# Kernel optimization log

Hardware: AMD Instinct MI355X
Metric: run time of the kernel (lower is better)

The kernel has to match this reference:

```python
import jax, jax.numpy as jnp
import numpy as np

NEI_SIZE = [16]  # matches init kwarg nei_size

def setup_inputs() -> dict:
    key = jax.random.key(0)
    k = jax.random.split(key, 5)
    B, N, S = 512, 32, 16
    EF, NF = 64, 128
    return {
        "x": jax.random.normal(k[0], (B, N, NF), dtype=jnp.float32),
        "x_nei_rel": jax.random.normal(k[1], (B, N * S, EF), dtype=jnp.float32),
        "x_nei_node": jax.random.normal(k[2], (B, N * S, NF), dtype=jnp.float32),
        "W1_w": jax.random.normal(k[3], (NF, EF + NF), dtype=jnp.float32) * 0.05,
        "W1_b": jax.random.normal(k[4], (NF,), dtype=jnp.float32) * 0.05,
        "i": 0,
    }

def reference(x, x_nei_rel, x_nei_node, W1_w, W1_b, i):
    S = NEI_SIZE[i]                       # now_nei_size (static python int)
    B, N, D = x.shape                     # N = n_neibor, D = nodeFea
    norm = 1.0 / np.sqrt(D).astype(np.float32)
    # concat edge+node feats and project: [B, N*S, EF+NF] -> [B, N*S, D]
    x_nei = jnp.concatenate([x_nei_rel, x_nei_node], axis=-1)
    v = (x_nei @ W1_w.T + W1_b).reshape(B, N, S, D)
    # per-node attention over its S neighbors
    alpha = jnp.einsum('bnd,bnsd->bns', x, v) * norm   # [B, N, S]
    alpha = jax.nn.softmax(alpha, axis=-1)
    # weighted neighbor sum
    return jnp.einsum('bns,bnsd->bnd', alpha, v)       # [B, N, D]
```

## Files before the change

### kernel.cpp

```cpp
#include <hip/hip_runtime.h>
#include <stdint.h>


typedef __attribute__((ext_vector_type(8))) short short8;
typedef __attribute__((ext_vector_type(4))) float float4_t;
typedef __attribute__((ext_vector_type(4))) unsigned short ushort4_t;

#define NBLK 2048
#define TILES_PER_BLK 8

__device__ __forceinline__ unsigned short f2bf(float f) {
    uint32_t u = __float_as_uint(f);
    u += 0x7fffu + ((u >> 16) & 1u);
    return (unsigned short)(u >> 16);
}

__device__ __forceinline__ int aoff(int s, int kc) {
    return (((kc >> 5) * 64) + (((kc & 31) >> 3) * 16) + s) * 8 + (kc & 7);
}

__global__ __launch_bounds__(128, 3) void nei_attn_kernel(
    const float* __restrict__ x,
    const float* __restrict__ rel,
    const float* __restrict__ node,
    const float* __restrict__ W,
    const float* __restrict__ bias,
    float* __restrict__ out)
{
    __shared__ __align__(16) unsigned short lds_f[6 * 64 * 8];
    __shared__ __align__(16) float lds_v[16][132];
    __shared__ float lds_alpha[2][16];
    __shared__ float lds_w[2][16];

    const int t    = threadIdx.x;
    const int lane = t & 63;
    const int wv   = t >> 6;
    const int l15  = lane & 15;
    const int quad = lane >> 4;

    short8 wfrag[4][6];
    #pragma unroll
    for (int dt = 0; dt < 4; ++dt) {
        const float* wr = W + (size_t)(64 * wv + dt * 16 + l15) * 192;
        #pragma unroll
        for (int q = 0; q < 6; ++q) {
            const float* p = wr + q * 32 + quad * 8;
            float4_t a = *(const float4_t*)p;
            float4_t b = *(const float4_t*)(p + 4);
            short8 f;
            f[0] = (short)f2bf(a.x); f[1] = (short)f2bf(a.y);
            f[2] = (short)f2bf(a.z); f[3] = (short)f2bf(a.w);
            f[4] = (short)f2bf(b.x); f[5] = (short)f2bf(b.y);
            f[6] = (short)f2bf(b.z); f[7] = (short)f2bf(b.w);
            wfrag[dt][q] = f;
        }
    }
    const float bias_l = bias[64 * wv + lane];

    const int s_st = wv * 8 + (lane & 7);
    const int fb   = lane >> 3;
    int ao[6];
    #pragma unroll
    for (int c = 0; c < 6; ++c) ao[c] = aoff(s_st, (fb + 8 * c) * 4);

    int tile = blockIdx.x * TILES_PER_BLK;
    for (int it = 0; it < TILES_PER_BLK; ++it, ++tile) {
        float4_t ld[6];
        {
            const float4_t* rb = (const float4_t*)rel  + (size_t)tile * 256 + s_st * 16;
            const float4_t* nb = (const float4_t*)node + (size_t)tile * 512 + s_st * 32;
            ld[0] = rb[fb];      ld[1] = rb[fb + 8];
            ld[2] = nb[fb];      ld[3] = nb[fb + 8];
            ld[4] = nb[fb + 16]; ld[5] = nb[fb + 24];
        }
        #pragma unroll
        for (int c = 0; c < 6; ++c) {
            ushort4_t u;
            u[0] = f2bf(ld[c].x); u[1] = f2bf(ld[c].y);
            u[2] = f2bf(ld[c].z); u[3] = f2bf(ld[c].w);
            *(ushort4_t*)&lds_f[ao[c]] = u;
        }
        __syncthreads();

        float4_t xv[4];
        #pragma unroll
        for (int dt = 0; dt < 4; ++dt)
            xv[dt] = *(const float4_t*)(x + (size_t)tile * 128 + 64 * wv + 16 * dt + 4 * quad);

        float4_t acc[4];
        #pragma unroll
        for (int dt = 0; dt < 4; ++dt) acc[dt] = (float4_t){0.f, 0.f, 0.f, 0.f};
        #pragma unroll
        for (int q = 0; q < 6; ++q) {
            short8 bfr = *(const short8*)&lds_f[(q * 64 + lane) * 8];
            #pragma unroll
            for (int dt = 0; dt < 4; ++dt)
                acc[dt] = __builtin_amdgcn_mfma_f32_16x16x32_bf16(wfrag[dt][q], bfr, acc[dt], 0, 0, 0);
        }

        float ap = 0.f;
        #pragma unroll
        for (int dt = 0; dt < 4; ++dt)
            ap += xv[dt].x * acc[dt][0] + xv[dt].y * acc[dt][1]
                + xv[dt].z * acc[dt][2] + xv[dt].w * acc[dt][3];
        ap += __shfl_xor(ap, 16);
        ap += __shfl_xor(ap, 32);
        if (lane < 16) lds_alpha[wv][lane] = ap;

        #pragma unroll
        for (int dt = 0; dt < 4; ++dt)
            *(float4_t*)&lds_v[l15][64 * wv + 16 * dt + 4 * quad] = acc[dt];

        __syncthreads();

        const float alpha = (ap + lds_alpha[1 - wv][l15]) * 0.08838834764831845f;
        float mx = alpha;
        mx = fmaxf(mx, __shfl_xor(mx, 1));
        mx = fmaxf(mx, __shfl_xor(mx, 2));
        mx = fmaxf(mx, __shfl_xor(mx, 4));
        mx = fmaxf(mx, __shfl_xor(mx, 8));
        const float e = __expf(alpha - mx);
        float den = e;
        den += __shfl_xor(den, 1);
        den += __shfl_xor(den, 2);
        den += __shfl_xor(den, 4);
        den += __shfl_xor(den, 8);
        const float wgt = e / den;
        if (quad == 0) lds_w[wv][l15] = wgt;

        const int md = 64 * wv + lane;
        float4_t w0 = *(const float4_t*)&lds_w[wv][0];
        float4_t w1 = *(const float4_t*)&lds_w[wv][4];
        float4_t w2 = *(const float4_t*)&lds_w[wv][8];
        float4_t w3 = *(const float4_t*)&lds_w[wv][12];
        float o = bias_l;
        o += w0.x * lds_v[0][md]  + w0.y * lds_v[1][md]
           + w0.z * lds_v[2][md]  + w0.w * lds_v[3][md];
        o += w1.x * lds_v[4][md]  + w1.y * lds_v[5][md]
           + w1.z * lds_v[6][md]  + w1.w * lds_v[7][md];
        o += w2.x * lds_v[8][md]  + w2.y * lds_v[9][md]
           + w2.z * lds_v[10][md] + w2.w * lds_v[11][md];
        o += w3.x * lds_v[12][md] + w3.y * lds_v[13][md]
           + w3.z * lds_v[14][md] + w3.w * lds_v[15][md];
        out[(size_t)tile * 128 + md] = o;
    }
}

extern "C" void kernel_launch(void* const* d_in, const int* in_sizes, int n_in,
                              void* d_out, int out_size, void* d_ws, size_t ws_size,
                              hipStream_t stream) {
    const float* x    = (const float*)d_in[0];
    const float* rel  = (const float*)d_in[1];
    const float* node = (const float*)d_in[2];
    const float* W    = (const float*)d_in[3];
    const float* bias = (const float*)d_in[4];
    float* out = (float*)d_out;
    hipLaunchKernelGGL(nei_attn_kernel, dim3(NBLK), dim3(128), 0, stream,
                       x, rel, node, W, bias, out);
}
```

Baseline: 299.7 us.

## Load MFMA B operands directly from global, prefetch next tile, use 4 waves

Drops the LDS staging of converted neighbour features. Each lane now loads its MFMA B fragment straight from global memory and converts it to bf16 in registers with packed conversion intrinsics. The block grows to 4 waves, each owning 32 output dims, which halves the per-thread W fragments and lets more waves hide latency. The next tile's loads are issued after the barrier, and LDS buffers are double-buffered to overlap memory with the softmax and weighted sum, at the cost of more live registers and one fewer barrier per tile.

```diff
diff --git a/kernel.cpp b/kernel.cpp
--- a/kernel.cpp
+++ b/kernel.cpp
@@ -1,25 +1,22 @@
 #include <hip/hip_runtime.h>
+#include <hip/hip_bf16.h>
 #include <stdint.h>
 
 
 typedef __attribute__((ext_vector_type(8))) short short8;
 typedef __attribute__((ext_vector_type(4))) float float4_t;
-typedef __attribute__((ext_vector_type(4))) unsigned short ushort4_t;
 
 #define NBLK 2048
 #define TILES_PER_BLK 8
 
-__device__ __forceinline__ unsigned short f2bf(float f) {
-    uint32_t u = __float_as_uint(f);
-    u += 0x7fffu + ((u >> 16) & 1u);
-    return (unsigned short)(u >> 16);
+__device__ __forceinline__ uint32_t pk2bf(float a, float b) {
+    __hip_bfloat162 h = __float22bfloat162_rn(float2{a, b});
+    union { __hip_bfloat162 h2; uint32_t u; } c;
+    c.h2 = h;
+    return c.u;
 }
 
-__device__ __forceinline__ int aoff(int s, int kc) {
-    return (((kc >> 5) * 64) + (((kc & 31) >> 3) * 16) + s) * 8 + (kc & 7);
-}
-
-__global__ __launch_bounds__(128, 3) void nei_attn_kernel(
+__global__ __launch_bounds__(256, 4) void nei_attn_kernel(
     const float* __restrict__ x,
     const float* __restrict__ rel,
     const float* __restrict__ node,
@@ -27,10 +24,9 @@
     const float* __restrict__ bias,
     float* __restrict__ out)
 {
-    __shared__ __align__(16) unsigned short lds_f[6 * 64 * 8];
-    __shared__ __align__(16) float lds_v[16][132];
-    __shared__ float lds_alpha[2][16];
-    __shared__ float lds_w[2][16];
+    __shared__ __align__(16) float lds_v[2][16][132];
+    __shared__ __align__(16) float lds_alpha[2][16][4];
+    __shared__ __align__(16) float lds_wgt[2][4][16];
 
     const int t    = threadIdx.x;
     const int lane = t & 63;
@@ -38,82 +34,81 @@
     const int l15  = lane & 15;
     const int quad = lane >> 4;
 
-    short8 wfrag[4][6];
+    short8 wfrag[2][6];
     #pragma unroll
-    for (int dt = 0; dt < 4; ++dt) {
-        const float* wr = W + (size_t)(64 * wv + dt * 16 + l15) * 192;
+    for (int dt = 0; dt < 2; ++dt) {
+        const float* wr = W + (size_t)(32 * wv + 16 * dt + l15) * 192 + quad * 8;
         #pragma unroll
         for (int q = 0; q < 6; ++q) {
-            const float* p = wr + q * 32 + quad * 8;
-            float4_t a = *(const float4_t*)p;
-            float4_t b = *(const float4_t*)(p + 4);
-            short8 f;
-            f[0] = (short)f2bf(a.x); f[1] = (short)f2bf(a.y);
-            f[2] = (short)f2bf(a.z); f[3] = (short)f2bf(a.w);
-            f[4] = (short)f2bf(b.x); f[5] = (short)f2bf(b.y);
-            f[6] = (short)f2bf(b.z); f[7] = (short)f2bf(b.w);
-            wfrag[dt][q] = f;
+            float4_t a = *(const float4_t*)(wr + 32 * q);
+            float4_t b = *(const float4_t*)(wr + 32 * q + 4);
+            union { uint32_t u[4]; short8 s; } f;
+            f.u[0] = pk2bf(a.x, a.y); f.u[1] = pk2bf(a.z, a.w);
+            f.u[2] = pk2bf(b.x, b.y); f.u[3] = pk2bf(b.z, b.w);
+            wfrag[dt][q] = f.s;
         }
     }
-    const float bias_l = bias[64 * wv + lane];
-
-    const int s_st = wv * 8 + (lane & 7);
-    const int fb   = lane >> 3;
-    int ao[6];
-    #pragma unroll
-    for (int c = 0; c < 6; ++c) ao[c] = aoff(s_st, (fb + 8 * c) * 4);
+    const float bias_l = bias[32 * wv + (lane & 31)];
 
     int tile = blockIdx.x * TILES_PER_BLK;
-    for (int it = 0; it < TILES_PER_BLK; ++it, ++tile) {
-        float4_t ld[6];
-        {
-            const float4_t* rb = (const float4_t*)rel  + (size_t)tile * 256 + s_st * 16;
-            const float4_t* nb = (const float4_t*)node + (size_t)tile * 512 + s_st * 32;
-            ld[0] = rb[fb];      ld[1] = rb[fb + 8];
-            ld[2] = nb[fb];      ld[3] = nb[fb + 8];
-            ld[4] = nb[fb + 16]; ld[5] = nb[fb + 24];
-        }
-        #pragma unroll
-        for (int c = 0; c < 6; ++c) {
-            ushort4_t u;
-            u[0] = f2bf(ld[c].x); u[1] = f2bf(ld[c].y);
-            u[2] = f2bf(ld[c].z); u[3] = f2bf(ld[c].w);
-            *(ushort4_t*)&lds_f[ao[c]] = u;
-        }
-        __syncthreads();
 
-        float4_t xv[4];
-        #pragma unroll
-        for (int dt = 0; dt < 4; ++dt)
-            xv[dt] = *(const float4_t*)(x + (size_t)tile * 128 + 64 * wv + 16 * dt + 4 * quad);
+    float4_t lda[6], ldb[6], xv0, xv1;
+    {
+        const float* fr = rel  + (size_t)tile * 1024 + l15 * 64  + quad * 8;
+        const float* fn = node + (size_t)tile * 2048 + l15 * 128 + quad * 8;
+        lda[0] = *(const float4_t*)(fr);       ldb[0] = *(const float4_t*)(fr + 4);
+        lda[1] = *(const float4_t*)(fr + 32);  ldb[1] = *(const float4_t*)(fr + 36);
+        lda[2] = *(const float4_t*)(fn);       ldb[2] = *(const float4_t*)(fn + 4);
+        lda[3] = *(const float4_t*)(fn + 32);  ldb[3] = *(const float4_t*)(fn + 36);
+        lda[4] = *(const float4_t*)(fn + 64);  ldb[4] = *(const float4_t*)(fn + 68);
+        lda[5] = *(const float4_t*)(fn + 96);  ldb[5] = *(const float4_t*)(fn + 100);
+        xv0 = *(const float4_t*)(x + (size_t)tile * 128 + 32 * wv + 4 * quad);
+        xv1 = *(const float4_t*)(x + (size_t)tile * 128 + 32 * wv + 16 + 4 * quad);
+    }
 
-        float4_t acc[4];
-        #pragma unroll
-        for (int dt = 0; dt < 4; ++dt) acc[dt] = (float4_t){0.f, 0.f, 0.f, 0.f};
+    for (int it = 0; it < TILES_PER_BLK; ++it) {
+        const int buf = it & 1;
+
+        float4_t acc0 = {0.f, 0.f, 0.f, 0.f};
+        float4_t acc1 = {0.f, 0.f, 0.f, 0.f};
         #pragma unroll
         for (int q = 0; q < 6; ++q) {
-            short8 bfr = *(const short8*)&lds_f[(q * 64 + lane) * 8];
-            #pragma unroll
-            for (int dt = 0; dt < 4; ++dt)
-                acc[dt] = __builtin_amdgcn_mfma_f32_16x16x32_bf16(wfrag[dt][q], bfr, acc[dt], 0, 0, 0);
+            union { uint32_t u[4]; short8 s; } f;
+            f.u[0] = pk2bf(lda[q].x, lda[q].y);
+            f.u[1] = pk2bf(lda[q].z, lda[q].w);
+            f.u[2] = pk2bf(ldb[q].x, ldb[q].y);
+            f.u[3] = pk2bf(ldb[q].z, ldb[q].w);
+            acc0 = __builtin_amdgcn_mfma_f32_16x16x32_bf16(wfrag[0][q], f.s, acc0, 0, 0, 0);
+            acc1 = __builtin_amdgcn_mfma_f32_16x16x32_bf16(wfrag[1][q], f.s, acc1, 0, 0, 0);
         }
 
-        float ap = 0.f;
-        #pragma unroll
-        for (int dt = 0; dt < 4; ++dt)
-            ap += xv[dt].x * acc[dt][0] + xv[dt].y * acc[dt][1]
-                + xv[dt].z * acc[dt][2] + xv[dt].w * acc[dt][3];
+        float ap = xv0.x * acc0[0] + xv0.y * acc0[1] + xv0.z * acc0[2] + xv0.w * acc0[3]
+                 + xv1.x * acc1[0] + xv1.y * acc1[1] + xv1.z * acc1[2] + xv1.w * acc1[3];
         ap += __shfl_xor(ap, 16);
         ap += __shfl_xor(ap, 32);
-        if (lane < 16) lds_alpha[wv][lane] = ap;
+        if (quad == 0) lds_alpha[buf][l15][wv] = ap;
 
-        #pragma unroll
-        for (int dt = 0; dt < 4; ++dt)
-            *(float4_t*)&lds_v[l15][64 * wv + 16 * dt + 4 * quad] = acc[dt];
+        *(float4_t*)&lds_v[buf][l15][32 * wv + 4 * quad]      = acc0;
+        *(float4_t*)&lds_v[buf][l15][32 * wv + 16 + 4 * quad] = acc1;
 
         __syncthreads();
 
-        const float alpha = (ap + lds_alpha[1 - wv][l15]) * 0.08838834764831845f;
+        if (it + 1 < TILES_PER_BLK) {
+            const int nt = tile + 1;
+            const float* fr = rel  + (size_t)nt * 1024 + l15 * 64  + quad * 8;
+            const float* fn = node + (size_t)nt * 2048 + l15 * 128 + quad * 8;
+            lda[0] = *(const float4_t*)(fr);       ldb[0] = *(const float4_t*)(fr + 4);
+            lda[1] = *(const float4_t*)(fr + 32);  ldb[1] = *(const float4_t*)(fr + 36);
+            lda[2] = *(const float4_t*)(fn);       ldb[2] = *(const float4_t*)(fn + 4);
+            lda[3] = *(const float4_t*)(fn + 32);  ldb[3] = *(const float4_t*)(fn + 36);
+            lda[4] = *(const float4_t*)(fn + 64);  ldb[4] = *(const float4_t*)(fn + 68);
+            lda[5] = *(const float4_t*)(fn + 96);  ldb[5] = *(const float4_t*)(fn + 100);
+            xv0 = *(const float4_t*)(x + (size_t)nt * 128 + 32 * wv + 4 * quad);
+            xv1 = *(const float4_t*)(x + (size_t)nt * 128 + 32 * wv + 16 + 4 * quad);
+        }
+
+        float4_t apv = *(const float4_t*)&lds_alpha[buf][l15][0];
+        const float alpha = (apv.x + apv.y + apv.z + apv.w) * 0.08838834764831845f;
         float mx = alpha;
         mx = fmaxf(mx, __shfl_xor(mx, 1));
         mx = fmaxf(mx, __shfl_xor(mx, 2));
@@ -126,23 +121,20 @@
         den += __shfl_xor(den, 4);
         den += __shfl_xor(den, 8);
         const float wgt = e / den;
-        if (quad == 0) lds_w[wv][l15] = wgt;
+        if (quad == 0) lds_wgt[buf][wv][l15] = wgt;
 
-        const int md = 64 * wv + lane;
-        float4_t w0 = *(const float4_t*)&lds_w[wv][0];
-        float4_t w1 = *(const float4_t*)&lds_w[wv][4];
-        float4_t w2 = *(const float4_t*)&lds_w[wv][8];
-        float4_t w3 = *(const float4_t*)&lds_w[wv][12];
-        float o = bias_l;
-        o += w0.x * lds_v[0][md]  + w0.y * lds_v[1][md]
-           + w0.z * lds_v[2][md]  + w0.w * lds_v[3][md];
-        o += w1.x * lds_v[4][md]  + w1.y * lds_v[5][md]
-           + w1.z * lds_v[6][md]  + w1.w * lds_v[7][md];
-        o += w2.x * lds_v[8][md]  + w2.y * lds_v[9][md]
-           + w2.z * lds_v[10][md] + w2.w * lds_v[11][md];
-        o += w3.x * lds_v[12][md] + w3.y * lds_v[13][md]
-           + w3.z * lds_v[14][md] + w3.w * lds_v[15][md];
-        out[(size_t)tile * 128 + md] = o;
+        const int dc = 32 * wv + (lane & 31);
+        const int sh = (lane >> 5) * 8;
+        float4_t wA = *(const float4_t*)&lds_wgt[buf][wv][sh];
+        float4_t wB = *(const float4_t*)&lds_wgt[buf][wv][sh + 4];
+        float o = wA.x * lds_v[buf][sh + 0][dc] + wA.y * lds_v[buf][sh + 1][dc]
+                + wA.z * lds_v[buf][sh + 2][dc] + wA.w * lds_v[buf][sh + 3][dc]
+                + wB.x * lds_v[buf][sh + 4][dc] + wB.y * lds_v[buf][sh + 5][dc]
+                + wB.z * lds_v[buf][sh + 6][dc] + wB.w * lds_v[buf][sh + 7][dc];
+        o += __shfl_xor(o, 32);
+        if (lane < 32) out[(size_t)tile * 128 + dc] = o + bias_l;
+
+        ++tile;
     }
 }
 
@@ -155,6 +147,6 @@
     const float* W    = (const float*)d_in[3];
     const float* bias = (const float*)d_in[4];
     float* out = (float*)d_out;
-    hipLaunchKernelGGL(nei_attn_kernel, dim3(NBLK), dim3(128), 0, stream,
+    hipLaunchKernelGGL(nei_attn_kernel, dim3(NBLK), dim3(256), 0, stream,
                        x, rel, node, W, bias, out);
 }
```

Measured after the change: 339.2 us. 13.2% more time.
